# Optimization experiments

Hardware: AMD Instinct MI355X
Metric: run time of the kernel (lower is better)

The kernel has to match this reference:

```python
import jax, jax.numpy as jnp
import numpy as np

# EdMIPS quantizer constants for 2-bit
HWGQ_STEP = 0.538      # hwgq_steps[2]
GAUSS_STEP = 0.996     # gaussian_steps[2]
ABIT = 2
WBIT = 2
BN_EPS = 1e-3


def setup_inputs() -> dict:
    key = jax.random.key(0)
    k1, k2 = jax.random.split(key, 2)
    x = jax.random.normal(k1, (32, 128, 56, 56), jnp.float32)
    gamma = jnp.ones((128,), jnp.float32)
    beta = jnp.zeros((128,), jnp.float32)
    weight = jax.random.normal(k2, (128, 128, 3, 3), jnp.float32) * 0.05
    return {"x": x, "gamma": gamma, "beta": beta, "weight": weight}


def _hwgq(x):
    # HWGQ: clamp to [0, step*(2^abit - 1)], then round to uniform levels.
    lvls = float(2 ** ABIT - 1)
    thr = HWGQ_STEP * lvls
    y = jnp.clip(x, 0.0, thr)
    q = jnp.round(y / HWGQ_STEP) * HWGQ_STEP
    # straight-through estimator: forward = q, backward = d/dy (clip mask)
    return y + jax.lax.stop_gradient(q - y)


def _gauss_quantize(w):
    # step scaled by weight std (detached, torch uses .item()); mid-rise quantizer.
    step = GAUSS_STEP * jax.lax.stop_gradient(jnp.std(w))
    lvls = float(2 ** WBIT) / 2.0
    q = (jnp.round(w / step + 0.5) - 0.5) * step
    thr = (lvls - 0.5) * step
    q = jnp.clip(q, -thr, thr)
    # full straight-through: backward = identity
    return w + jax.lax.stop_gradient(q - w)


def reference(x, gamma, beta, weight):
    # BatchNorm2d (training-mode batch stats, biased variance, eps=0.001)
    mean = jnp.mean(x, axis=(0, 2, 3), keepdims=True)
    var = jnp.var(x, axis=(0, 2, 3), keepdims=True)
    xn = (x - mean) * jax.lax.rsqrt(var + BN_EPS)
    xn = xn * gamma[None, :, None, None] + beta[None, :, None, None]
    # quantized activations and weights, then plain conv (bias=False)
    a = _hwgq(xn)
    qw = _gauss_quantize(weight)
    out = jax.lax.conv_general_dilated(
        a, qw,
        window_strides=(1, 1),
        padding=((1, 1), (1, 1)),
        dimension_numbers=("NCHW", "OIHW", "NCHW"),
    )
    return out  # [32, 128, 56, 56]
```

## Files before the change

### kernel.cpp

```cpp
#include <hip/hip_runtime.h>

typedef int i32x4 __attribute__((ext_vector_type(4)));

#define C_IN 128
#define HW 56
#define PIX 3136
#define NPLANE 401408
#define PROWB 7424
#define APAD_NSTRIDE 430592

static __device__ __forceinline__ void gload_lds16(const void* g, void* l) {
  __builtin_amdgcn_global_load_lds((__attribute__((address_space(1))) unsigned int*)g,
                                   (__attribute__((address_space(3))) unsigned int*)l, 16, 0, 0);
}

__global__ __launch_bounds__(256) void stats_k(const float* __restrict__ x,
                                               const float* __restrict__ w,
                                               double* __restrict__ bnpart,
                                               double* __restrict__ wpart) {
  const int b = blockIdx.x, tid = threadIdx.x;
  double s = 0.0, s2 = 0.0;
  if (b < 1024) {
    const int c = b & 127, sl = b >> 7;
    for (int n = sl * 4; n < sl * 4 + 4; ++n) {
      const float4* p = (const float4*)(x + (size_t)(n * C_IN + c) * PIX);
      for (int i = tid; i < PIX / 4; i += 256) {
        float4 v = p[i];
        s  += (double)v.x + (double)v.y + (double)v.z + (double)v.w;
        s2 += (double)v.x * v.x + (double)v.y * v.y + (double)v.z * v.z + (double)v.w * v.w;
      }
    }
  } else {
    const int wb = b - 1024;
    const float4* p = (const float4*)w;
    for (int i = wb * 576 + tid; i < (wb + 1) * 576; i += 256) {
      float4 v = p[i];
      s  += (double)v.x + (double)v.y + (double)v.z + (double)v.w;
      s2 += (double)v.x * v.x + (double)v.y * v.y + (double)v.z * v.z + (double)v.w * v.w;
    }
  }
  __shared__ double red[8];
  const int lane = tid & 63, wv = tid >> 6;
  for (int off = 32; off; off >>= 1) { s += __shfl_down(s, off); s2 += __shfl_down(s2, off); }
  if (lane == 0) { red[wv * 2] = s; red[wv * 2 + 1] = s2; }
  __syncthreads();
  if (tid == 0) {
    double* dst = (b < 1024) ? (bnpart + ((b & 127) * 8 + (b >> 7)) * 2)
                             : (wpart + (b - 1024) * 2);
    dst[0] = red[0] + red[2] + red[4] + red[6];
    dst[1] = red[1] + red[3] + red[5] + red[7];
  }
}

__global__ __launch_bounds__(256) void quant_k(const float* __restrict__ x,
                                               const float* __restrict__ w,
                                               const float* __restrict__ gamma,
                                               const float* __restrict__ beta,
                                               const double* __restrict__ bnpart,
                                               const double* __restrict__ wpart,
                                               signed char* __restrict__ apad,
                                               signed char* __restrict__ wq,
                                               float* __restrict__ stepp) {
  const int tid = threadIdx.x;
  if (blockIdx.y == 32) {
    const int bx = blockIdx.x;
    __shared__ float steps;
    __shared__ __align__(16) signed char wl[3 * 1152];
    if (tid < 64) {
      double s = wpart[tid * 2], s2 = wpart[tid * 2 + 1];
      for (int off = 32; off; off >>= 1) { s += __shfl_down(s, off); s2 += __shfl_down(s2, off); }
      if (tid == 0) {
        const double mean = s / 147456.0;
        const double var = s2 / 147456.0 - mean * mean;
        steps = 0.996f * (float)sqrt(var);
        if (bx == 0) stepp[0] = steps;
      }
    }
    __syncthreads();
    const float step = steps;
    for (int i = tid; i < 3456; i += 256) {
      const int oi = i / 1152, rem = i - oi * 1152;
      const int oc = bx + oi * 58;
      if (oc < 128) {
        const int c = rem / 9, rs = rem - c * 9;
        const float v = w[(size_t)(oc * C_IN + c) * 9 + rs];
        float t = 2.f * rintf(v / step + 0.5f) - 1.f;
        t = fminf(fmaxf(t, -3.f), 3.f);
        wl[oi * 1152 + rs * 128 + c] = (signed char)(int)t;
      }
    }
    __syncthreads();
    for (int i = tid; i < 216; i += 256) {
      const int oi = i / 72, rem = i - oi * 72;
      const int oc = bx + oi * 58;
      if (oc < 128) {
        const int rs = rem >> 3, c16 = rem & 7;
        *(uint4*)(wq + rs * 16384 + ((oc * 128 + c16 * 16) ^ ((oc & 7) << 4))) =
            *(const uint4*)(wl + oi * 1152 + rs * 128 + c16 * 16);
      }
    }
    return;
  }
  const int hh = blockIdx.x;
  const int n = blockIdx.y;
  __shared__ float2 aff[128];
  __shared__ __align__(16) signed char lds[58 * 144];
  if (tid < 128) {
    double s = 0.0, s2 = 0.0;
    for (int i = 0; i < 8; ++i) { s += bnpart[(tid * 8 + i) * 2]; s2 += bnpart[(tid * 8 + i) * 2 + 1]; }
    const double mean = s / 100352.0;
    const double var = s2 / 100352.0 - mean * mean;
    const double inv = 1.0 / sqrt(var + 1e-3);
    aff[tid] = make_float2((float)((double)gamma[tid] * inv),
                           (float)((double)beta[tid] - mean * inv * (double)gamma[tid]));
  }
  uint4* lds4 = (uint4*)lds;
  for (int i = tid; i < 58 * 144 / 16; i += 256) lds4[i] = make_uint4(0, 0, 0, 0);
  __syncthreads();
  if (hh >= 1 && hh <= 56) {
    const float* xp = x + (size_t)n * NPLANE + (hh - 1) * HW;
    for (int i = tid; i < C_IN * HW; i += 256) {
      const int ww = i % HW, c = i / HW;
      const float v = xp[(size_t)c * PIX + ww];
      const float2 af = aff[c];
      const float xn = fmaf(v, af.x, af.y);
      const float y = fminf(fmaxf(xn, 0.f), 1.614f);
      lds[(ww + 1) * 144 + c] = (signed char)(int)rintf(y * (1.f / 0.538f));
    }
  }
  __syncthreads();
  signed char* dst = apad + (size_t)n * APAD_NSTRIDE;
  for (int i = tid; i < 58 * 8; i += 256) {
    const int col = i >> 3, c16 = i & 7;
    const int pp = hh * 58 + col;
    *(uint4*)(dst + (((size_t)pp * 128 + c16 * 16) ^ ((pp & 7) << 4))) = lds4[col * 9 + c16];
  }
}

__global__ __launch_bounds__(256, 2) void conv_k(const signed char* __restrict__ apad,
                                                 const signed char* __restrict__ wq,
                                                 const float* __restrict__ stepp,
                                                 float* __restrict__ out) {
  __shared__ __align__(16) signed char Al[45056];
  __shared__ __align__(16) signed char Wl[2][16384];
  const int bid = blockIdx.x;
  const int vid = (bid & 7) * 56 + (bid >> 3);
  const int n = vid / 14;
  const int rg = vid - n * 14;
  const int tid = threadIdx.x;
  const int wv = tid >> 6, lane = tid & 63;
  const int lr = lane & 15, q4 = lane >> 4;
  const int kq = q4 * 16;
  const int ohalf = (wv & 1) * 64;
  const int phalf = (wv >> 1) * 112;

  {
    const signed char* gsrc = apad + (size_t)n * APAD_NSTRIDE + (size_t)(rg * 4) * PROWB;
    for (int i = wv; i < 44; i += 4)
      gload_lds16(gsrc + i * 1024 + lane * 16, Al + i * 1024);
  }
  for (int i = wv; i < 16; i += 4)
    gload_lds16(wq + i * 1024 + lane * 16, &Wl[0][i * 1024]);

  int pbase[7];
#pragma unroll
  for (int pf = 0; pf < 7; ++pf) {
    const int po = phalf + pf * 16 + lr;
    pbase[pf] = (po / 56) * 58 + po % 56;
  }

  i32x4 acc[7][4];
#pragma unroll
  for (int i = 0; i < 7; ++i)
#pragma unroll
    for (int j = 0; j < 4; ++j) acc[i][j] = (i32x4){0, 0, 0, 0};

  __syncthreads();

  for (int rs = 0; rs < 9; ++rs) {
    if (rs < 8) {
      for (int i = wv; i < 16; i += 4)
        gload_lds16(wq + (rs + 1) * 16384 + i * 1024 + lane * 16, &Wl[(rs + 1) & 1][i * 1024]);
    }
    const int r = rs / 3, s = rs - 3 * r;
    const int poff = r * 58 + s;
    const signed char* Wb = Wl[rs & 1];
#pragma unroll
    for (int k64 = 0; k64 < 2; ++k64) {
      const int kb = k64 * 64 + kq;
      i32x4 wf[4];
#pragma unroll
      for (int of = 0; of < 4; ++of) {
        const int row = ohalf + of * 16 + lr;
        wf[of] = *(const i32x4*)(Wb + row * 128 + (kb ^ ((row & 7) << 4)));
      }
#pragma unroll
      for (int pf = 0; pf < 7; ++pf) {
        const int p = pbase[pf] + poff;
        const i32x4 bf = *(const i32x4*)(Al + p * 128 + (kb ^ ((p & 7) << 4)));
        acc[pf][0] = __builtin_amdgcn_mfma_i32_16x16x64_i8(wf[0], bf, acc[pf][0], 0, 0, 0);
        acc[pf][1] = __builtin_amdgcn_mfma_i32_16x16x64_i8(wf[1], bf, acc[pf][1], 0, 0, 0);
        acc[pf][2] = __builtin_amdgcn_mfma_i32_16x16x64_i8(wf[2], bf, acc[pf][2], 0, 0, 0);
        acc[pf][3] = __builtin_amdgcn_mfma_i32_16x16x64_i8(wf[3], bf, acc[pf][3], 0, 0, 0);
      }
    }
    if (rs < 8) __syncthreads();
  }

  const float oscale = 0.269f * stepp[0];
  float* outn = out + (size_t)n * NPLANE + (size_t)rg * 224;
#pragma unroll
  for (int pf = 0; pf < 7; ++pf) {
    const int po = phalf + pf * 16 + lr;
    float* op = outn + po;
#pragma unroll
    for (int of = 0; of < 4; ++of) {
      const int oc = ohalf + of * 16 + q4 * 4;
#pragma unroll
      for (int q = 0; q < 4; ++q)
        op[(size_t)(oc + q) * PIX] = (float)acc[pf][of][q] * oscale;
    }
  }
}

extern "C" void kernel_launch(void* const* d_in, const int* in_sizes, int n_in,
                              void* d_out, int out_size, void* d_ws, size_t ws_size,
                              hipStream_t stream) {
  const float* x = (const float*)d_in[0];
  const float* gamma = (const float*)d_in[1];
  const float* beta = (const float*)d_in[2];
  const float* w = (const float*)d_in[3];
  float* out = (float*)d_out;
  char* ws = (char*)d_ws;

  double* bnpart = (double*)(ws);
  double* wpart = (double*)(ws + 16384);
  float* stepp = (float*)(ws + 17408);
  signed char* wq = (signed char*)(ws + 18432);
  signed char* apad = (signed char*)(ws + 196608);

  stats_k<<<1088, 256, 0, stream>>>(x, w, bnpart, wpart);
  quant_k<<<dim3(58, 33), 256, 0, stream>>>(x, w, gamma, beta, bnpart, wpart, apad, wq, stepp);
  conv_k<<<448, 256, 0, stream>>>(apad, wq, stepp, out);
}
```

Measured before the change: 52.84 us.

## Fuse activation BN+quantization into conv kernel and read weights from global

Drops the separate activation-quantize pass and the padded int8 staging buffer. The conv kernel now builds the normalized 2-bit activations for its six input rows straight from fp32 x into LDS, including the halo zeros. Weight quantization moves to a small separate kernel, and the conv reads weight fragments directly from global memory instead of double-buffering them through LDS, which also removes the per-tap barriers. The trade-off is that adjacent row groups re-read overlapping x rows, and weight loads now depend on cache latency rather than LDS.

```diff
diff --git a/kernel.cpp b/kernel.cpp
--- a/kernel.cpp
+++ b/kernel.cpp
@@ -6,13 +6,6 @@
 #define HW 56
 #define PIX 3136
 #define NPLANE 401408
-#define PROWB 7424
-#define APAD_NSTRIDE 430592
-
-static __device__ __forceinline__ void gload_lds16(const void* g, void* l) {
-  __builtin_amdgcn_global_load_lds((__attribute__((address_space(1))) unsigned int*)g,
-                                   (__attribute__((address_space(3))) unsigned int*)l, 16, 0, 0);
-}
 
 __global__ __launch_bounds__(256) void stats_k(const float* __restrict__ x,
                                                const float* __restrict__ w,
@@ -52,97 +45,48 @@
   }
 }
 
-__global__ __launch_bounds__(256) void quant_k(const float* __restrict__ x,
-                                               const float* __restrict__ w,
-                                               const float* __restrict__ gamma,
-                                               const float* __restrict__ beta,
-                                               const double* __restrict__ bnpart,
-                                               const double* __restrict__ wpart,
-                                               signed char* __restrict__ apad,
-                                               signed char* __restrict__ wq,
-                                               float* __restrict__ stepp) {
-  const int tid = threadIdx.x;
-  if (blockIdx.y == 32) {
-    const int bx = blockIdx.x;
-    __shared__ float steps;
-    __shared__ __align__(16) signed char wl[3 * 1152];
-    if (tid < 64) {
-      double s = wpart[tid * 2], s2 = wpart[tid * 2 + 1];
-      for (int off = 32; off; off >>= 1) { s += __shfl_down(s, off); s2 += __shfl_down(s2, off); }
-      if (tid == 0) {
-        const double mean = s / 147456.0;
-        const double var = s2 / 147456.0 - mean * mean;
-        steps = 0.996f * (float)sqrt(var);
-        if (bx == 0) stepp[0] = steps;
-      }
-    }
-    __syncthreads();
-    const float step = steps;
-    for (int i = tid; i < 3456; i += 256) {
-      const int oi = i / 1152, rem = i - oi * 1152;
-      const int oc = bx + oi * 58;
-      if (oc < 128) {
-        const int c = rem / 9, rs = rem - c * 9;
-        const float v = w[(size_t)(oc * C_IN + c) * 9 + rs];
-        float t = 2.f * rintf(v / step + 0.5f) - 1.f;
-        t = fminf(fmaxf(t, -3.f), 3.f);
-        wl[oi * 1152 + rs * 128 + c] = (signed char)(int)t;
-      }
-    }
-    __syncthreads();
-    for (int i = tid; i < 216; i += 256) {
-      const int oi = i / 72, rem = i - oi * 72;
-      const int oc = bx + oi * 58;
-      if (oc < 128) {
-        const int rs = rem >> 3, c16 = rem & 7;
-        *(uint4*)(wq + rs * 16384 + ((oc * 128 + c16 * 16) ^ ((oc & 7) << 4))) =
-            *(const uint4*)(wl + oi * 1152 + rs * 128 + c16 * 16);
-      }
-    }
-    return;
-  }
-  const int hh = blockIdx.x;
-  const int n = blockIdx.y;
-  __shared__ float2 aff[128];
-  __shared__ __align__(16) signed char lds[58 * 144];
-  if (tid < 128) {
-    double s = 0.0, s2 = 0.0;
-    for (int i = 0; i < 8; ++i) { s += bnpart[(tid * 8 + i) * 2]; s2 += bnpart[(tid * 8 + i) * 2 + 1]; }
-    const double mean = s / 100352.0;
-    const double var = s2 / 100352.0 - mean * mean;
-    const double inv = 1.0 / sqrt(var + 1e-3);
-    aff[tid] = make_float2((float)((double)gamma[tid] * inv),
-                           (float)((double)beta[tid] - mean * inv * (double)gamma[tid]));
-  }
-  uint4* lds4 = (uint4*)lds;
-  for (int i = tid; i < 58 * 144 / 16; i += 256) lds4[i] = make_uint4(0, 0, 0, 0);
-  __syncthreads();
-  if (hh >= 1 && hh <= 56) {
-    const float* xp = x + (size_t)n * NPLANE + (hh - 1) * HW;
-    for (int i = tid; i < C_IN * HW; i += 256) {
-      const int ww = i % HW, c = i / HW;
-      const float v = xp[(size_t)c * PIX + ww];
-      const float2 af = aff[c];
-      const float xn = fmaf(v, af.x, af.y);
-      const float y = fminf(fmaxf(xn, 0.f), 1.614f);
-      lds[(ww + 1) * 144 + c] = (signed char)(int)rintf(y * (1.f / 0.538f));
-    }
-  }
-  __syncthreads();
-  signed char* dst = apad + (size_t)n * APAD_NSTRIDE;
-  for (int i = tid; i < 58 * 8; i += 256) {
-    const int col = i >> 3, c16 = i & 7;
-    const int pp = hh * 58 + col;
-    *(uint4*)(dst + (((size_t)pp * 128 + c16 * 16) ^ ((pp & 7) << 4))) = lds4[col * 9 + c16];
-  }
-}
-
-__global__ __launch_bounds__(256, 2) void conv_k(const signed char* __restrict__ apad,
+__global__ __launch_bounds__(128) void quant_w_k(const float* __restrict__ w,
+                                                 const double* __restrict__ wpart,
+                                                 signed char* __restrict__ wq,
+                                                 float* __restrict__ stepp) {
+  const int oc = blockIdx.x, tid = threadIdx.x;
+  __shared__ float steps;
+  __shared__ __align__(16) signed char lds[9 * 128];
+  if (tid < 64) {
+    double s = wpart[tid * 2], s2 = wpart[tid * 2 + 1];
+    for (int off = 32; off; off >>= 1) { s += __shfl_down(s, off); s2 += __shfl_down(s2, off); }
+    if (tid == 0) {
+      const double mean = s / 147456.0;
+      const double var = s2 / 147456.0 - mean * mean;
+      steps = 0.996f * (float)sqrt(var);
+      if (oc == 0) stepp[0] = steps;
+    }
+  }
+  __syncthreads();
+  const float step = steps;
+  for (int i = tid; i < 1152; i += 128) {
+    const int c = i / 9, rs = i - c * 9;
+    const float v = w[(size_t)(oc * C_IN + c) * 9 + rs];
+    float t = 2.f * rintf(v / step + 0.5f) - 1.f;
+    t = fminf(fmaxf(t, -3.f), 3.f);
+    lds[rs * 128 + c] = (signed char)(int)t;
+  }
+  __syncthreads();
+  for (int i = tid; i < 72; i += 128) {
+    const int rs = i >> 3, c16 = i & 7;
+    *(uint4*)(wq + rs * 16384 + oc * 128 + c16 * 16) = *(const uint4*)(lds + rs * 128 + c16 * 16);
+  }
+}
+
+__global__ __launch_bounds__(256, 2) void conv_k(const float* __restrict__ x,
+                                                 const double* __restrict__ bnpart,
+                                                 const float* __restrict__ gamma,
+                                                 const float* __restrict__ beta,
                                                  const signed char* __restrict__ wq,
                                                  const float* __restrict__ stepp,
                                                  float* __restrict__ out) {
   __shared__ __align__(16) signed char Al[45056];
-  __shared__ __align__(16) signed char Wl[2][16384];
+  __shared__ float2 aff[128];
   const int bid = blockIdx.x;
   const int vid = (bid & 7) * 56 + (bid >> 3);
   const int n = vid / 14;
@@ -154,13 +98,53 @@
   const int ohalf = (wv & 1) * 64;
   const int phalf = (wv >> 1) * 112;
 
-  {
-    const signed char* gsrc = apad + (size_t)n * APAD_NSTRIDE + (size_t)(rg * 4) * PROWB;
-    for (int i = wv; i < 44; i += 4)
-      gload_lds16(gsrc + i * 1024 + lane * 16, Al + i * 1024);
-  }
-  for (int i = wv; i < 16; i += 4)
-    gload_lds16(wq + i * 1024 + lane * 16, &Wl[0][i * 1024]);
+  if (tid < 128) {
+    double s = 0.0, s2 = 0.0;
+    for (int i = 0; i < 8; ++i) { s += bnpart[(tid * 8 + i) * 2]; s2 += bnpart[(tid * 8 + i) * 2 + 1]; }
+    const double mean = s / 100352.0;
+    const double var = s2 / 100352.0 - mean * mean;
+    const double inv = 1.0 / sqrt(var + 1e-3);
+    aff[tid] = make_float2((float)((double)gamma[tid] * inv),
+                           (float)((double)beta[tid] - mean * inv * (double)gamma[tid]));
+  }
+  const uint4 z4 = make_uint4(0, 0, 0, 0);
+  if (tid < 96) {
+    const int j = tid >> 4, rem = tid & 15;
+    const int px = j * 58 + (rem >> 3) * 57;
+    *(uint4*)(Al + (((px * 128) + (rem & 7) * 16) ^ ((px & 7) << 4))) = z4;
+  }
+  if (rg == 0)
+    for (int i = tid; i < 448; i += 256) {
+      const int px = 1 + (i >> 3);
+      *(uint4*)(Al + ((px * 128 + (i & 7) * 16) ^ ((px & 7) << 4))) = z4;
+    }
+  if (rg == 13)
+    for (int i = tid; i < 448; i += 256) {
+      const int px = 5 * 58 + 1 + (i >> 3);
+      *(uint4*)(Al + ((px * 128 + (i & 7) * 16) ^ ((px & 7) << 4))) = z4;
+    }
+  __syncthreads();
+
+  for (int j = 0; j < 6; ++j) {
+    const int hp = rg * 4 + j;
+    if (hp < 1 || hp > 56) continue;
+    const float* xrowb = x + (size_t)n * NPLANE + (size_t)(hp - 1) * HW;
+    for (int i = tid; i < 1792; i += 256) {
+      const int c4 = i / 56, w = i - c4 * 56;
+      const float* xp = xrowb + (size_t)(c4 * 4) * PIX + w;
+      unsigned int pack = 0;
+#pragma unroll
+      for (int k = 0; k < 4; ++k) {
+        const float2 af = aff[c4 * 4 + k];
+        const float xn = fmaf(xp[(size_t)k * PIX], af.x, af.y);
+        const float y = fminf(fmaxf(xn, 0.f), 1.614f);
+        pack |= (unsigned int)(int)rintf(y * (1.f / 0.538f)) << (8 * k);
+      }
+      const int px = j * 58 + 1 + w;
+      *(unsigned int*)(Al + ((px * 128 + c4 * 4) ^ ((px & 7) << 4))) = pack;
+    }
+  }
+  __syncthreads();
 
   int pbase[7];
 #pragma unroll
@@ -175,36 +159,27 @@
 #pragma unroll
     for (int j = 0; j < 4; ++j) acc[i][j] = (i32x4){0, 0, 0, 0};
 
-  __syncthreads();
-
   for (int rs = 0; rs < 9; ++rs) {
-    if (rs < 8) {
-      for (int i = wv; i < 16; i += 4)
-        gload_lds16(wq + (rs + 1) * 16384 + i * 1024 + lane * 16, &Wl[(rs + 1) & 1][i * 1024]);
-    }
     const int r = rs / 3, s = rs - 3 * r;
     const int poff = r * 58 + s;
-    const signed char* Wb = Wl[rs & 1];
+    const signed char* wrow = wq + rs * 16384;
 #pragma unroll
     for (int k64 = 0; k64 < 2; ++k64) {
       const int kb = k64 * 64 + kq;
       i32x4 wf[4];
 #pragma unroll
-      for (int of = 0; of < 4; ++of) {
-        const int row = ohalf + of * 16 + lr;
-        wf[of] = *(const i32x4*)(Wb + row * 128 + (kb ^ ((row & 7) << 4)));
-      }
+      for (int of = 0; of < 4; ++of)
+        wf[of] = *(const i32x4*)(wrow + (ohalf + of * 16 + lr) * 128 + kb);
 #pragma unroll
       for (int pf = 0; pf < 7; ++pf) {
         const int p = pbase[pf] + poff;
-        const i32x4 bf = *(const i32x4*)(Al + p * 128 + (kb ^ ((p & 7) << 4)));
+        const i32x4 bf = *(const i32x4*)(Al + ((p * 128 + kb) ^ ((p & 7) << 4)));
         acc[pf][0] = __builtin_amdgcn_mfma_i32_16x16x64_i8(wf[0], bf, acc[pf][0], 0, 0, 0);
         acc[pf][1] = __builtin_amdgcn_mfma_i32_16x16x64_i8(wf[1], bf, acc[pf][1], 0, 0, 0);
         acc[pf][2] = __builtin_amdgcn_mfma_i32_16x16x64_i8(wf[2], bf, acc[pf][2], 0, 0, 0);
         acc[pf][3] = __builtin_amdgcn_mfma_i32_16x16x64_i8(wf[3], bf, acc[pf][3], 0, 0, 0);
       }
     }
-    if (rs < 8) __syncthreads();
   }
 
   const float oscale = 0.269f * stepp[0];
@@ -237,9 +212,8 @@
   double* wpart = (double*)(ws + 16384);
   float* stepp = (float*)(ws + 17408);
   signed char* wq = (signed char*)(ws + 18432);
-  signed char* apad = (signed char*)(ws + 196608);
 
   stats_k<<<1088, 256, 0, stream>>>(x, w, bnpart, wpart);
-  quant_k<<<dim3(58, 33), 256, 0, stream>>>(x, w, gamma, beta, bnpart, wpart, apad, wq, stepp);
-  conv_k<<<448, 256, 0, stream>>>(apad, wq, stepp, out);
-}
+  quant_w_k<<<128, 128, 0, stream>>>(w, wpart, wq, stepp);
+  conv_k<<<448, 256, 0, stream>>>(x, bnpart, gamma, beta, wq, stepp, out);
+}
```

New measurement: 63.43 us. 20.0% more time.

## Read quantized weights directly from global memory in conv, drop LDS weight staging

Applied to the files above, without the earlier changes.

The conv kernel no longer double-buffers weight tiles in LDS. Weight fragments are now loaded straight from global memory, where the small 147KB weight array should stay cached, and the per-tap __syncthreads are removed. The weight swizzle is dropped to match, the loop is unrolled by 3, and the activation tail load is trimmed so the prefetch stays within the array. Separately, the quantize kernel now reads x as float4. Less LDS per block and no barriers may help overlap, but each wave now does global/L2 loads inside the MFMA loop, which adds latency risk.

```diff
diff --git a/kernel.cpp b/kernel.cpp
--- a/kernel.cpp
+++ b/kernel.cpp
@@ -95,7 +95,7 @@
       const int oc = bx + oi * 58;
       if (oc < 128) {
         const int rs = rem >> 3, c16 = rem & 7;
-        *(uint4*)(wq + rs * 16384 + ((oc * 128 + c16 * 16) ^ ((oc & 7) << 4))) =
+        *(uint4*)(wq + rs * 16384 + oc * 128 + c16 * 16) =
             *(const uint4*)(wl + oi * 1152 + rs * 128 + c16 * 16);
       }
     }
@@ -119,13 +119,15 @@
   __syncthreads();
   if (hh >= 1 && hh <= 56) {
     const float* xp = x + (size_t)n * NPLANE + (hh - 1) * HW;
-    for (int i = tid; i < C_IN * HW; i += 256) {
-      const int ww = i % HW, c = i / HW;
-      const float v = xp[(size_t)c * PIX + ww];
+    for (int i = tid; i < 1792; i += 256) {
+      const int c = i / 14, w4 = (i - c * 14) * 4;
+      const float4 v = *(const float4*)(xp + (size_t)c * PIX + w4);
       const float2 af = aff[c];
-      const float xn = fmaf(v, af.x, af.y);
-      const float y = fminf(fmaxf(xn, 0.f), 1.614f);
-      lds[(ww + 1) * 144 + c] = (signed char)(int)rintf(y * (1.f / 0.538f));
+      const float k = 1.f / 0.538f;
+      lds[(w4 + 1) * 144 + c] = (signed char)(int)rintf(fminf(fmaxf(fmaf(v.x, af.x, af.y), 0.f), 1.614f) * k);
+      lds[(w4 + 2) * 144 + c] = (signed char)(int)rintf(fminf(fmaxf(fmaf(v.y, af.x, af.y), 0.f), 1.614f) * k);
+      lds[(w4 + 3) * 144 + c] = (signed char)(int)rintf(fminf(fmaxf(fmaf(v.z, af.x, af.y), 0.f), 1.614f) * k);
+      lds[(w4 + 4) * 144 + c] = (signed char)(int)rintf(fminf(fmaxf(fmaf(v.w, af.x, af.y), 0.f), 1.614f) * k);
     }
   }
   __syncthreads();
@@ -142,7 +144,6 @@
                                                  const float* __restrict__ stepp,
                                                  float* __restrict__ out) {
   __shared__ __align__(16) signed char Al[45056];
-  __shared__ __align__(16) signed char Wl[2][16384];
   const int bid = blockIdx.x;
   const int vid = (bid & 7) * 56 + (bid >> 3);
   const int n = vid / 14;
@@ -157,10 +158,9 @@
   {
     const signed char* gsrc = apad + (size_t)n * APAD_NSTRIDE + (size_t)(rg * 4) * PROWB;
     for (int i = wv; i < 44; i += 4)
-      gload_lds16(gsrc + i * 1024 + lane * 16, Al + i * 1024);
-  }
-  for (int i = wv; i < 16; i += 4)
-    gload_lds16(wq + i * 1024 + lane * 16, &Wl[0][i * 1024]);
+      if (i < 43 || lane < 32)
+        gload_lds16(gsrc + i * 1024 + lane * 16, Al + i * 1024);
+  }
 
   int pbase[7];
 #pragma unroll
@@ -177,34 +177,28 @@
 
   __syncthreads();
 
+#pragma unroll 3
   for (int rs = 0; rs < 9; ++rs) {
-    if (rs < 8) {
-      for (int i = wv; i < 16; i += 4)
-        gload_lds16(wq + (rs + 1) * 16384 + i * 1024 + lane * 16, &Wl[(rs + 1) & 1][i * 1024]);
-    }
     const int r = rs / 3, s = rs - 3 * r;
     const int poff = r * 58 + s;
-    const signed char* Wb = Wl[rs & 1];
+    const signed char* wrow = wq + rs * 16384;
 #pragma unroll
     for (int k64 = 0; k64 < 2; ++k64) {
       const int kb = k64 * 64 + kq;
       i32x4 wf[4];
 #pragma unroll
-      for (int of = 0; of < 4; ++of) {
-        const int row = ohalf + of * 16 + lr;
-        wf[of] = *(const i32x4*)(Wb + row * 128 + (kb ^ ((row & 7) << 4)));
-      }
+      for (int of = 0; of < 4; ++of)
+        wf[of] = *(const i32x4*)(wrow + (ohalf + of * 16 + lr) * 128 + kb);
 #pragma unroll
       for (int pf = 0; pf < 7; ++pf) {
         const int p = pbase[pf] + poff;
-        const i32x4 bf = *(const i32x4*)(Al + p * 128 + (kb ^ ((p & 7) << 4)));
+        const i32x4 bf = *(const i32x4*)(Al + ((p * 128 + kb) ^ ((p & 7) << 4)));
         acc[pf][0] = __builtin_amdgcn_mfma_i32_16x16x64_i8(wf[0], bf, acc[pf][0], 0, 0, 0);
         acc[pf][1] = __builtin_amdgcn_mfma_i32_16x16x64_i8(wf[1], bf, acc[pf][1], 0, 0, 0);
         acc[pf][2] = __builtin_amdgcn_mfma_i32_16x16x64_i8(wf[2], bf, acc[pf][2], 0, 0, 0);
         acc[pf][3] = __builtin_amdgcn_mfma_i32_16x16x64_i8(wf[3], bf, acc[pf][3], 0, 0, 0);
       }
     }
-    if (rs < 8) __syncthreads();
   }
 
   const float oscale = 0.269f * stepp[0];
```

Measured after the change: 59.43 us. 12.5% more time.
